# Kernel tuning notes

Measured on AMD Instinct MI355X. Metric: run time of the kernel, lower is better.

The kernel has to match this reference:

```python
import jax, jax.numpy as jnp
import numpy as np
from jax.experimental.ode import odeint

OBS_DIM, LATENT_DIM, HIDDEN_DIM = 64, 3, 128
T, B = 200, 4096
NUM_ENCODE = 50
DYN_H = 100


def setup_inputs() -> dict:
    key = jax.random.key(0)
    ks = jax.random.split(key, 20)
    def rn(k, shape, fan_in):
        return (jax.random.normal(k, shape, jnp.float32) / np.float32(np.sqrt(fan_in)))
    return {
        "observations": jax.random.normal(ks[0], (T, B, OBS_DIM), jnp.float32),
        "epsilon": jax.random.normal(ks[1], (B, LATENT_DIM), jnp.float32),
        # GRU params (PyTorch layout: W_ih [3H, in], W_hh [3H, H])
        "gru_Wih": rn(ks[2], (3 * HIDDEN_DIM, OBS_DIM), OBS_DIM),
        "gru_Whh": rn(ks[3], (3 * HIDDEN_DIM, HIDDEN_DIM), HIDDEN_DIM),
        "gru_bih": jnp.zeros((3 * HIDDEN_DIM,), jnp.float32),
        "gru_bhh": jnp.zeros((3 * HIDDEN_DIM,), jnp.float32),
        "mean_W": rn(ks[4], (LATENT_DIM, HIDDEN_DIM), HIDDEN_DIM),
        "mean_b": jnp.zeros((LATENT_DIM,), jnp.float32),
        "logvar_W": rn(ks[5], (LATENT_DIM, HIDDEN_DIM), HIDDEN_DIM),
        "logvar_b": jnp.zeros((LATENT_DIM,), jnp.float32),
        # dynamics MLP 3->100->100->3
        "dyn_W1": rn(ks[6], (DYN_H, LATENT_DIM), LATENT_DIM),
        "dyn_b1": jnp.zeros((DYN_H,), jnp.float32),
        "dyn_W2": rn(ks[7], (DYN_H, DYN_H), DYN_H),
        "dyn_b2": jnp.zeros((DYN_H,), jnp.float32),
        "dyn_W3": rn(ks[8], (LATENT_DIM, DYN_H), DYN_H),
        "dyn_b3": jnp.zeros((LATENT_DIM,), jnp.float32),
        # decoder MLP latent->64->obs
        "dec_W1": rn(ks[9], (64, LATENT_DIM), LATENT_DIM),
        "dec_b1": jnp.zeros((64,), jnp.float32),
        "dec_W2": rn(ks[10], (OBS_DIM, 64), 64),
        "dec_b2": jnp.zeros((OBS_DIM,), jnp.float32),
        "time_steps": jnp.arange(T, dtype=jnp.float32) * jnp.float32(0.01),
    }


def _gru_last(x, Wih, Whh, bih, bhh):
    # x: [T, B, obs_dim]; PyTorch GRU cell math, zero initial state
    H = Whh.shape[1]
    def step(h, xt):
        gi = xt @ Wih.T + bih          # [B, 3H]
        gh = h @ Whh.T + bhh           # [B, 3H]
        i_r, i_z, i_n = jnp.split(gi, 3, axis=-1)
        h_r, h_z, h_n = jnp.split(gh, 3, axis=-1)
        r = jax.nn.sigmoid(i_r + h_r)
        z = jax.nn.sigmoid(i_z + h_z)
        n = jnp.tanh(i_n + r * h_n)
        return (1.0 - z) * n + z * h, None
    h0 = jnp.zeros((x.shape[1], H), x.dtype)
    h_last, _ = jax.lax.scan(step, h0, x)
    return h_last


def reference(observations, epsilon, gru_Wih, gru_Whh, gru_bih, gru_bhh,
              mean_W, mean_b, logvar_W, logvar_b,
              dyn_W1, dyn_b1, dyn_W2, dyn_b2, dyn_W3, dyn_b3,
              dec_W1, dec_b1, dec_W2, dec_b2, time_steps):
    h_last = _gru_last(observations[:NUM_ENCODE], gru_Wih, gru_Whh, gru_bih, gru_bhh)
    z0_mean = h_last @ mean_W.T + mean_b
    z0_logvar = h_last @ logvar_W.T + logvar_b
    std = jnp.exp(0.5 * z0_logvar)
    z0 = z0_mean + epsilon * std

    def dyn(z, t):
        h = jnp.tanh(z @ dyn_W1.T + dyn_b1)
        h = jnp.tanh(h @ dyn_W2.T + dyn_b2)
        return h @ dyn_W3.T + dyn_b3

    # dopri5 adaptive solver (torchdiffeq default tolerances)
    traj = odeint(dyn, z0, time_steps, rtol=1e-7, atol=1e-9)  # [T, B, latent]
    h = jax.nn.relu(traj @ dec_W1.T + dec_b1)
    recon = h @ dec_W2.T + dec_b2                              # [T, B, obs]
    return recon, z0_mean, z0_logvar, traj
```

## Files before the change

### kernel.cpp

```cpp
#include <hip/hip_runtime.h>
#include <stddef.h>

#define OFF_MEAN 52428800
#define OFF_LV   52441088
#define OFF_TRAJ 52453376

typedef _Float16 f16x8 __attribute__((ext_vector_type(8)));
typedef _Float16 f16x4 __attribute__((ext_vector_type(4)));
typedef float    f32x4 __attribute__((ext_vector_type(4)));

#define MFMA16(a, b, c) __builtin_amdgcn_mfma_f32_16x16x32_f16((a), (b), (c), 0, 0, 0)

__device__ __forceinline__ float sigm_(float x) {
    float e = __builtin_amdgcn_exp2f(x * -1.442695041f);
    return __builtin_amdgcn_rcpf(1.f + e);
}
__device__ __forceinline__ float tanh_(float x) {
    float e = __builtin_amdgcn_exp2f(x * 2.885390082f);
    return 1.f - 2.f * __builtin_amdgcn_rcpf(e + 1.f);
}
__device__ __forceinline__ float dot4_(float4 a, float4 b) {
    return a.x * b.x + a.y * b.y + a.z * b.z + a.w * b.w;
}

__global__ __launch_bounds__(512, 2) void k_gru(
    const float* __restrict__ obs, const float* __restrict__ eps,
    const float* __restrict__ Wih, const float* __restrict__ Whh,
    const float* __restrict__ bih, const float* __restrict__ bhh,
    const float* __restrict__ meanW, const float* __restrict__ meanB,
    const float* __restrict__ lvW,  const float* __restrict__ lvB,
    float* __restrict__ o_mean, float* __restrict__ o_lv, float* __restrict__ z0)
{
    __shared__ alignas(16) unsigned short h_s[2][2048];
    __shared__ alignas(16) unsigned short x_s[2][1024];
    __shared__ alignas(16) float hm_s[16 * 132];
    __shared__ float mb_s[96];

    const int tid  = threadIdx.x;
    const int b0   = blockIdx.x * 16;
    const int lane = tid & 63, wv = tid >> 6;
    const int lrow = lane & 15, lkb = lane >> 4;
    const int swX  = (lrow & 7) << 4;
    const int swH  = lrow << 4;
    const int u    = wv * 16 + lrow;

    const float bR  = bih[u]       + bhh[u];
    const float bZ  = bih[128 + u] + bhh[128 + u];
    const float bNi = bih[256 + u];
    const float bNh = bhh[256 + u];

    f16x8 wihf[3][2];
    #pragma unroll
    for (int g = 0; g < 3; ++g) {
        int col = g * 128 + u;
        #pragma unroll
        for (int ks = 0; ks < 2; ++ks) {
            const float* wp = Wih + col * 64 + ks * 32 + lkb * 8;
            float4 a = *(const float4*)wp, b = *(const float4*)(wp + 4);
            float tmp[8] = {a.x, a.y, a.z, a.w, b.x, b.y, b.z, b.w};
            f16x8 hv;
            #pragma unroll
            for (int j = 0; j < 8; ++j) hv[j] = (_Float16)tmp[j];
            wihf[g][ks] = hv;
        }
    }
    f16x8 whhh[3][4];
    #pragma unroll
    for (int g = 0; g < 3; ++g) {
        int col = g * 128 + u;
        #pragma unroll
        for (int ks = 0; ks < 4; ++ks) {
            const float* wp = Whh + col * 128 + ks * 32 + lkb * 8;
            float4 a = *(const float4*)wp, b = *(const float4*)(wp + 4);
            float tmp[8] = {a.x, a.y, a.z, a.w, b.x, b.y, b.z, b.w};
            f16x8 hv;
            #pragma unroll
            for (int j = 0; j < 8; ++j) hv[j] = (_Float16)tmp[j];
            whhh[g][ks] = hv;
        }
    }

    for (int i = tid; i < 2048; i += 512) h_s[0][i] = 0;
    const int srow = tid >> 4, skq = (tid & 15) * 4;
    const int sxb  = srow * 128 + ((skq * 2) ^ ((srow & 7) << 4));
    float4 xn;
    if (tid < 256) {
        xn = *(const float4*)(obs + ((size_t)0 * 4096 + b0 + srow) * 64 + skq);
        f16x4 vh = {(_Float16)xn.x, (_Float16)xn.y, (_Float16)xn.z, (_Float16)xn.w};
        *(f16x4*)((char*)x_s[0] + sxb) = vh;
    }
    f32x4 hold = {0.f, 0.f, 0.f, 0.f};
    __syncthreads();

    for (int t = 0; t < 50; ++t) {
        const int cur = t & 1, nxt = cur ^ 1;
        char* x_c = (char*)x_s[cur];
        char* h_c = (char*)h_s[cur];

        if (tid < 256) {
            int tt = (t < 49) ? t + 1 : t;
            xn = *(const float4*)(obs + ((size_t)tt * 4096 + b0 + srow) * 64 + skq);
        }

        f16x8 xh[2], hh[4];
        #pragma unroll
        for (int ks = 0; ks < 2; ++ks) {
            int off = lrow * 128 + ((ks * 64 + lkb * 16) ^ swX);
            xh[ks] = *(const f16x8*)(x_c + off);
        }
        #pragma unroll
        for (int ks = 0; ks < 4; ++ks) {
            int off = lrow * 256 + ((ks * 64 + lkb * 16) ^ swH);
            hh[ks] = *(const f16x8*)(h_c + off);
        }

        f32x4 z4 = {0.f, 0.f, 0.f, 0.f};
        f32x4 aR = z4, aZ = z4, aNi = z4, aNh = z4;
        #pragma unroll
        for (int ks = 0; ks < 2; ++ks) {
            aR  = MFMA16(xh[ks], wihf[0][ks], aR);
            aZ  = MFMA16(xh[ks], wihf[1][ks], aZ);
            aNi = MFMA16(xh[ks], wihf[2][ks], aNi);
        }
        #pragma unroll
        for (int ks = 0; ks < 4; ++ks) {
            aR  = MFMA16(hh[ks], whhh[0][ks], aR);
            aZ  = MFMA16(hh[ks], whhh[1][ks], aZ);
            aNh = MFMA16(hh[ks], whhh[2][ks], aNh);
        }

        char* hn_c = (char*)h_s[nxt];
        #pragma unroll
        for (int i = 0; i < 4; ++i) {
            float rg = sigm_(aR[i] + bR);
            float zg = sigm_(aZ[i] + bZ);
            float n  = tanh_(aNi[i] + bNi + rg * (aNh[i] + bNh));
            float hv = (1.f - zg) * n + zg * hold[i];
            hold[i] = hv;
            int ri = lkb * 4 + i;
            int hb = ri * 256 + ((u * 2) ^ (ri << 4));
            *(_Float16*)(hn_c + hb) = (_Float16)hv;
        }

        if (tid < 256 && t < 49) {
            f16x4 vh = {(_Float16)xn.x, (_Float16)xn.y, (_Float16)xn.z, (_Float16)xn.w};
            *(f16x4*)((char*)x_s[nxt] + sxb) = vh;
        }
        __syncthreads();
    }

    #pragma unroll
    for (int i = 0; i < 4; ++i)
        hm_s[(lkb * 4 + i) * 132 + u] = hold[i];
    __syncthreads();

    if (tid < 96) {
        int rr = tid / 6, c = tid - rr * 6, j = (c < 3) ? c : c - 3;
        const float* W = (c < 3) ? meanW : lvW;
        const float* B = (c < 3) ? meanB : lvB;
        float acc = B[j];
        const float4* W4 = (const float4*)(W + j * 128);
        const float4* h4 = (const float4*)(hm_s + rr * 132);
        #pragma unroll 4
        for (int kc = 0; kc < 32; ++kc) acc += dot4_(W4[kc], h4[kc]);
        mb_s[rr * 6 + c] = acc;
    }
    __syncthreads();
    if (tid < 48) {
        int rr = tid / 3, j = tid - rr * 3;
        int gb = b0 + rr;
        float m  = mb_s[rr * 6 + j];
        float lv = mb_s[rr * 6 + j + 3];
        o_mean[gb * 3 + j] = m;
        o_lv[gb * 3 + j]   = lv;
        z0[gb * 3 + j]     = m + eps[gb * 3 + j] * __expf(0.5f * lv);
    }
}

__global__ __launch_bounds__(256, 2) void k_odec(
    const float* __restrict__ dW1, const float* __restrict__ db1,
    const float* __restrict__ dW2, const float* __restrict__ db2,
    const float* __restrict__ dW3, const float* __restrict__ db3,
    const float* __restrict__ decW1, const float* __restrict__ decb1,
    const float* __restrict__ decW2, const float* __restrict__ decb2,
    const float* __restrict__ z0, float* __restrict__ traj, float* __restrict__ recon)
{
    __shared__ alignas(16) unsigned short h1_s[2048];
    __shared__ alignas(16) unsigned short hd_s[10240];
    __shared__ alignas(16) float h2f[8 * 104];
    __shared__ alignas(16) float W3s[312];
    __shared__ alignas(16) float zbuf[160 * 4];
    __shared__ float w1ds[192], b1ds[64];
    __shared__ float b2s[100], b3s[3];
    __shared__ float fparts[24];

    const int tid  = threadIdx.x;
    const int b0   = blockIdx.x * 8;
    const int lane = tid & 63, wv = tid >> 6;
    const int r    = tid >> 5;
    const int lrow = lane & 15, lkb = lane >> 4;
    const int swA  = (lrow & 7) << 4;
    char* h1c = (char*)h1_s;
    char* hdc = (char*)hd_s;

    for (int i = tid; i < 512; i += 256)
        ((unsigned int*)(h1c + 2048))[i] = 0u;
    if (tid < 32) h2f[(tid >> 2) * 104 + 100 + (tid & 3)] = 0.f;
    for (int i = tid; i < 312; i += 256) {
        int j = i / 104, k = i - j * 104;
        W3s[i] = (k < 100) ? dW3[j * 100 + k] : 0.f;
    }
    if (tid < 100) b2s[tid] = db2[tid];
    if (tid < 3)   b3s[tid] = db3[tid];
    if (tid < 192) w1ds[tid] = decW1[tid];
    if (tid < 64)  b1ds[tid] = decb1[tid];

    float w1r[12], b1r[4];
    {
        int k0q = (tid & 31) * 4;
        #pragma unroll
        for (int i = 0; i < 4; ++i) {
            int k = k0q + i;
            if (k < 100) {
                w1r[3 * i + 0] = dW1[k * 3 + 0];
                w1r[3 * i + 1] = dW1[k * 3 + 1];
                w1r[3 * i + 2] = dW1[k * 3 + 2];
                b1r[i] = db1[k];
            } else {
                w1r[3 * i + 0] = 0.f; w1r[3 * i + 1] = 0.f; w1r[3 * i + 2] = 0.f;
                b1r[i] = 0.f;
            }
        }
    }
    f16x8 w2h[2][4];
    #pragma unroll
    for (int tile = 0; tile < 2; ++tile) {
        int col = (wv * 2 + tile) * 16 + lrow;
        #pragma unroll
        for (int ks = 0; ks < 4; ++ks) {
            f16x8 hv;
            #pragma unroll
            for (int j = 0; j < 8; ++j) {
                int k = ks * 32 + lkb * 8 + j;
                float v = (col < 100 && k < 100) ? dW2[col * 100 + k] : 0.f;
                hv[j] = (_Float16)v;
            }
            w2h[tile][ks] = hv;
        }
    }
    const int colD = wv * 16 + lrow;
    f16x8 dbh[2];
    #pragma unroll
    for (int ks = 0; ks < 2; ++ks) {
        const float* wp = decW2 + colD * 64 + ks * 32 + lkb * 8;
        float4 a = *(const float4*)wp, b = *(const float4*)(wp + 4);
        float tmp[8] = {a.x, a.y, a.z, a.w, b.x, b.y, b.z, b.w};
        f16x8 hv;
        #pragma unroll
        for (int j = 0; j < 8; ++j) hv[j] = (_Float16)tmp[j];
        dbh[ks] = hv;
    }
    const float dbo = decb2[colD];

    float yv0 = z0[(b0 + r) * 3 + 0];
    float yv1 = z0[(b0 + r) * 3 + 1];
    float yv2 = z0[(b0 + r) * 3 + 2];
    float fc0, fc1, fc2;
    float k10, k11, k12, ka0, ka1, ka2, yn0, yn1, yn2;
    float po0 = 0.f, po1 = 0.f, po2 = 0.f;
    float pk0 = 0.f, pk1 = 0.f, pk2 = 0.f;
    float pn0 = 0.f, pn1 = 0.f, pn2 = 0.f;
    float pf0 = 0.f, pf1 = 0.f, pf2 = 0.f;
    int have = 0, pt0 = 0;
    __syncthreads();

#define ZCHUNK(T0_, HH_, INVN_)                                                   \
    do {                                                                          \
        for (int ii = (tid & 31); ii < 60; ii += 32) {                            \
            int q = ii / 3, j = ii - q * 3;                                       \
            float ysj = (j == 0) ? po0 : (j == 1) ? po1 : po2;                    \
            float f0j = (j == 0) ? pk0 : (j == 1) ? pk1 : pk2;                    \
            float ynj = (j == 0) ? pn0 : (j == 1) ? pn1 : pn2;                    \
            float fnj = (j == 0) ? pf0 : (j == 1) ? pf1 : pf2;                    \
            float th  = (float)q * (INVN_);                                       \
            float th2 = th * th, th3 = th2 * th;                                  \
            float ca = 2.f * th3 - 3.f * th2 + 1.f;                               \
            float cb = th3 - 2.f * th2 + th;                                      \
            float cc = 3.f * th2 - 2.f * th3;                                     \
            float cd = th3 - th2;                                                 \
            float v = ca * ysj + cb * (HH_) * f0j + cc * ynj + cd * (HH_) * fnj;  \
            traj[((size_t)((T0_) + q) * 4096 + b0 + r) * 3 + j] = v;              \
            zbuf[(q * 8 + r) * 4 + j] = v;                                        \
        }                                                                         \
    } while (0)

#define HCHUNK0                                                                   \
    do {                                                                          \
        const int p  = tid >> 1;                                                  \
        const int u0 = (tid & 1) * 32;                                            \
        const float z0v = zbuf[p * 4 + 0], z1v = zbuf[p * 4 + 1], z2v = zbuf[p * 4 + 2]; \
        const int sw = (p & 7) << 4;                                              \
        _Pragma("unroll")                                                         \
        for (int c = 0; c < 8; ++c) {                                             \
            f16x4 hh_;                                                            \
            _Pragma("unroll")                                                     \
            for (int i = 0; i < 4; ++i) {                                         \
                int u = u0 + c * 4 + i;                                           \
                float acc = b1ds[u] + w1ds[u * 3 + 0] * z0v                       \
                          + w1ds[u * 3 + 1] * z1v + w1ds[u * 3 + 2] * z2v;        \
                hh_[i] = (_Float16)fmaxf(acc, 0.f);                               \
            }                                                                     \
            int off = p * 128 + (((u0 + c * 4) * 2) ^ sw);                        \
            *(f16x4*)(hdc + off) = hh_;                                           \
        }                                                                         \
    } while (0)

#define HCHUNK1                                                                   \
    do {                                                                          \
        const int p  = 128 + (tid >> 3);                                          \
        const int u0 = (tid & 7) * 8;                                             \
        const float z0v = zbuf[p * 4 + 0], z1v = zbuf[p * 4 + 1], z2v = zbuf[p * 4 + 2]; \
        const int sw = (p & 7) << 4;                                              \
        _Pragma("unroll")                                                         \
        for (int c = 0; c < 2; ++c) {                                             \
            f16x4 hh_;                                                            \
            _Pragma("unroll")                                                     \
            for (int i = 0; i < 4; ++i) {                                         \
                int u = u0 + c * 4 + i;                                           \
                float acc = b1ds[u] + w1ds[u * 3 + 0] * z0v                       \
                          + w1ds[u * 3 + 1] * z1v + w1ds[u * 3 + 2] * z2v;        \
                hh_[i] = (_Float16)fmaxf(acc, 0.f);                               \
            }                                                                     \
            int off = p * 128 + (((u0 + c * 4) * 2) ^ sw);                        \
            *(f16x4*)(hdc + off) = hh_;                                           \
        }                                                                         \
    } while (0)

#define MCHUNK(PART_, T0_)                                                        \
    do {                                                                          \
        _Pragma("unroll")                                                         \
        for (int rt2 = 0; rt2 < 5; ++rt2) {                                       \
            int rt = (PART_) * 5 + rt2;                                           \
            int base = (rt * 16 + lrow) * 128;                                    \
            f16x8 a0 = *(const f16x8*)(hdc + base + ((lkb * 16) ^ swA));          \
            f16x8 a1 = *(const f16x8*)(hdc + base + ((64 + lkb * 16) ^ swA));     \
            f32x4 acc = {0.f, 0.f, 0.f, 0.f};                                     \
            acc = MFMA16(a0, dbh[0], acc);                                        \
            acc = MFMA16(a1, dbh[1], acc);                                        \
            _Pragma("unroll")                                                     \
            for (int i = 0; i < 4; ++i) {                                         \
                int pr = rt * 16 + lkb * 4 + i;                                   \
                int q2 = pr >> 3, row2 = pr & 7;                                  \
                recon[((size_t)((T0_) + q2) * 4096 + b0 + row2) * 64 + colD] = acc[i] + dbo; \
            }                                                                     \
        }                                                                         \
    } while (0)

#define FEVAL(Y0, Y1, Y2, CH)                                                     \
    do {                                                                          \
        {                                                            \
            int k0q = (tid & 31) * 4;                                             \
            f16x4 hA;                                                             \
            _Pragma("unroll")                                                     \
            for (int i = 0; i < 4; ++i) {                                         \
                float a_ = b1r[i] + w1r[3 * i] * (Y0)                             \
                         + w1r[3 * i + 1] * (Y1) + w1r[3 * i + 2] * (Y2);         \
                hA[i] = (_Float16)tanh_(a_);                                      \
            }                                                                     \
            *(f16x4*)(h1c + r * 256 + ((k0q * 2) ^ (r << 4))) = hA;               \
        }                                                                         \
        if (have) {                                                               \
            if ((CH) == 1) ZCHUNK(pt0, 0.20f, 0.05f);                             \
            else if ((CH) == 2) HCHUNK0;                                          \
            else if ((CH) == 3) { HCHUNK1; MCHUNK(0, pt0); }                      \
            else if ((CH) == 4) MCHUNK(1, pt0);                                   \
        }                                                                         \
        __syncthreads();                                                          \
        {                                                        \
            f16x8 ah[4];                                                          \
            _Pragma("unroll")                                                     \
            for (int ks = 0; ks < 4; ++ks)                                        \
                ah[ks] = *(const f16x8*)(h1c + lrow * 256 + ((ks * 64 + lkb * 16) ^ swA)); \
            f32x4 acc0 = {0.f, 0.f, 0.f, 0.f}, acc1 = {0.f, 0.f, 0.f, 0.f};       \
            _Pragma("unroll")                                                     \
            for (int ks = 0; ks < 4; ++ks) {                                      \
                acc0 = MFMA16(ah[ks], w2h[0][ks], acc0);                          \
                acc1 = MFMA16(ah[ks], w2h[1][ks], acc1);                          \
            }                                                                     \
            if (lkb < 2) {                                                        \
                int r0 = lkb * 4;                                                 \
                _Pragma("unroll")                                                 \
                for (int tile = 0; tile < 2; ++tile) {                            \
                    int col = (wv * 2 + tile) * 16 + lrow;                        \
                    f32x4 a = tile ? acc1 : acc0;                                 \
                    if (col < 100) {                                              \
                        float bb = b2s[col];                                      \
                        _Pragma("unroll")                                         \
                        for (int i = 0; i < 4; ++i)                               \
                            h2f[(r0 + i) * 104 + col] = tanh_(a[i] + bb);         \
                    }                                                             \
                }                                                                 \
            }                                                                     \
        }                                                                         \
        __syncthreads();                                                          \
        {                                  \
            if (tid < 192) {                                                      \
                int rr = tid / 24, rem = tid - rr * 24, j = rem >> 3, qc = rem & 7;\
                const float4* Wj = (const float4*)(W3s + j * 104);                \
                const float4* Hr = (const float4*)(h2f + rr * 104);               \
                float acc = 0.f;                                                  \
                _Pragma("unroll")                                                 \
                for (int kc = 0; kc < 4; ++kc) {                                  \
                    int k = qc + kc * 8;                                          \
                    if (k < 26) acc += dot4_(Wj[k], Hr[k]);                       \
                }                                                                 \
                acc += __shfl_xor(acc, 1);                                        \
                acc += __shfl_xor(acc, 2);                                        \
                acc += __shfl_xor(acc, 4);                                        \
                if (qc == 0) fparts[rr * 3 + j] = acc + b3s[j];                   \
            }                                                                     \
        }                                                                         \
        __syncthreads();                                                          \
        fc0 = fparts[r * 3 + 0];                                                  \
        fc1 = fparts[r * 3 + 1];                                                  \
        fc2 = fparts[r * 3 + 2];                                                  \
    } while (0)

    FEVAL(yv0, yv1, yv2, 0);

    #pragma unroll 1
    for (int s = 0; s < 10; ++s) {
        const float hh = (s < 9) ? 0.20f : 0.19f;
        have = (s >= 1);
        pt0  = (s - 1) * 20;

        k10 = fc0; k11 = fc1; k12 = fc2;
        ka0 = fc0; ka1 = fc1; ka2 = fc2;
        float yt0 = yv0 + 0.5f * hh * fc0, yt1 = yv1 + 0.5f * hh * fc1, yt2 = yv2 + 0.5f * hh * fc2;
        FEVAL(yt0, yt1, yt2, 1);
        ka0 += 2.f * fc0; ka1 += 2.f * fc1; ka2 += 2.f * fc2;
        yt0 = yv0 + 0.5f * hh * fc0; yt1 = yv1 + 0.5f * hh * fc1; yt2 = yv2 + 0.5f * hh * fc2;
        FEVAL(yt0, yt1, yt2, 2);
        ka0 += 2.f * fc0; ka1 += 2.f * fc1; ka2 += 2.f * fc2;
        yt0 = yv0 + hh * fc0; yt1 = yv1 + hh * fc1; yt2 = yv2 + hh * fc2;
        FEVAL(yt0, yt1, yt2, 3);
        ka0 += fc0; ka1 += fc1; ka2 += fc2;
        const float h6 = hh * (1.f / 6.f);
        yn0 = yv0 + h6 * ka0; yn1 = yv1 + h6 * ka1; yn2 = yv2 + h6 * ka2;
        FEVAL(yn0, yn1, yn2, 4);

        po0 = yv0; po1 = yv1; po2 = yv2;
        pk0 = k10; pk1 = k11; pk2 = k12;
        pn0 = yn0; pn1 = yn1; pn2 = yn2;
        pf0 = fc0; pf1 = fc1; pf2 = fc2;
        yv0 = yn0; yv1 = yn1; yv2 = yn2;
    }

    ZCHUNK(180, 0.19f, (1.f / 19.f));
    __syncthreads();
    HCHUNK0;
    HCHUNK1;
    __syncthreads();
    MCHUNK(0, 180);
    MCHUNK(1, 180);
#undef FEVAL
#undef ZCHUNK
#undef HCHUNK0
#undef HCHUNK1
#undef MCHUNK
}

extern "C" void kernel_launch(void* const* d_in, const int* in_sizes, int n_in,
                              void* d_out, int out_size, void* d_ws, size_t ws_size,
                              hipStream_t stream)
{
    const float* obs   = (const float*)d_in[0];
    const float* eps   = (const float*)d_in[1];
    const float* Wih   = (const float*)d_in[2];
    const float* Whh   = (const float*)d_in[3];
    const float* bih   = (const float*)d_in[4];
    const float* bhh   = (const float*)d_in[5];
    const float* meanW = (const float*)d_in[6];
    const float* meanB = (const float*)d_in[7];
    const float* lvW   = (const float*)d_in[8];
    const float* lvB   = (const float*)d_in[9];
    const float* dW1   = (const float*)d_in[10];
    const float* db1   = (const float*)d_in[11];
    const float* dW2   = (const float*)d_in[12];
    const float* db2   = (const float*)d_in[13];
    const float* dW3   = (const float*)d_in[14];
    const float* db3   = (const float*)d_in[15];
    const float* decW1 = (const float*)d_in[16];
    const float* decb1 = (const float*)d_in[17];
    const float* decW2 = (const float*)d_in[18];
    const float* decb2 = (const float*)d_in[19];

    float* out   = (float*)d_out;
    float* recon = out;
    float* omean = out + OFF_MEAN;
    float* olv   = out + OFF_LV;
    float* traj  = out + OFF_TRAJ;
    float* z0    = (float*)d_ws;

    k_gru<<<dim3(256), dim3(512), 0, stream>>>(obs, eps, Wih, Whh, bih, bhh,
                                               meanW, meanB, lvW, lvB, omean, olv, z0);
    k_odec<<<dim3(512), dim3(256), 0, stream>>>(dW1, db1, dW2, db2, dW3, db3,
                                                decW1, decb1, decW2, decb2,
                                                z0, traj, recon);
}
```

Baseline: 145.9 us.

## Restructure GRU kernel to 8 rows per block with 4 waves covering two hidden tiles

The GRU kernel now uses 256-thread blocks, each handling 8 batch rows instead of 16, and launches 512 blocks so more CUs get work. Each wave owns two 16-unit hidden slices, which doubles its per-wave weight registers and MFMA count, while half the MFMA rows are padding (zeroed) since only 8 rows are valid. The intent is to spread the sequential 50-step recurrence across more blocks and shorten the per-block dependency chain. The cost is wasted MFMA work on padded rows and higher register pressure per thread.

Result: slower. 200.2 us (+37.2%).

```diff
diff --git a/kernel.cpp b/kernel.cpp
--- a/kernel.cpp
+++ b/kernel.cpp
@@ -23,7 +23,7 @@
     return a.x * b.x + a.y * b.y + a.z * b.z + a.w * b.w;
 }
 
-__global__ __launch_bounds__(512, 2) void k_gru(
+__global__ __launch_bounds__(256, 2) void k_gru(
     const float* __restrict__ obs, const float* __restrict__ eps,
     const float* __restrict__ Wih, const float* __restrict__ Whh,
     const float* __restrict__ bih, const float* __restrict__ bhh,
@@ -33,63 +33,86 @@
 {
     __shared__ alignas(16) unsigned short h_s[2][2048];
     __shared__ alignas(16) unsigned short x_s[2][1024];
-    __shared__ alignas(16) float hm_s[16 * 132];
-    __shared__ float mb_s[96];
+    __shared__ alignas(16) float hm_s[8 * 132];
+    __shared__ float mb_s[48];
 
     const int tid  = threadIdx.x;
-    const int b0   = blockIdx.x * 16;
+    const int b0   = blockIdx.x * 8;
     const int lane = tid & 63, wv = tid >> 6;
     const int lrow = lane & 15, lkb = lane >> 4;
     const int swX  = (lrow & 7) << 4;
     const int swH  = lrow << 4;
-    const int u    = wv * 16 + lrow;
-
-    const float bR  = bih[u]       + bhh[u];
-    const float bZ  = bih[128 + u] + bhh[128 + u];
-    const float bNi = bih[256 + u];
-    const float bNh = bhh[256 + u];
-
-    f16x8 wihf[3][2];
-    #pragma unroll
-    for (int g = 0; g < 3; ++g) {
-        int col = g * 128 + u;
-        #pragma unroll
-        for (int ks = 0; ks < 2; ++ks) {
-            const float* wp = Wih + col * 64 + ks * 32 + lkb * 8;
-            float4 a = *(const float4*)wp, b = *(const float4*)(wp + 4);
-            float tmp[8] = {a.x, a.y, a.z, a.w, b.x, b.y, b.z, b.w};
-            f16x8 hv;
+    const int ua   = wv * 16 + lrow;
+    const int ub   = (wv + 4) * 16 + lrow;
+
+    float bRv[2], bZv[2], bNiv[2], bNhv[2];
+    {
+        const int us[2] = {ua, ub};
+        #pragma unroll
+        for (int s2 = 0; s2 < 2; ++s2) {
+            int u = us[s2];
+            bRv[s2]  = bih[u]       + bhh[u];
+            bZv[s2]  = bih[128 + u] + bhh[128 + u];
+            bNiv[s2] = bih[256 + u];
+            bNhv[s2] = bhh[256 + u];
+        }
+    }
+    f16x8 wihf[2][3][2];
+    {
+        const int us[2] = {ua, ub};
+        #pragma unroll
+        for (int s2 = 0; s2 < 2; ++s2) {
             #pragma unroll
-            for (int j = 0; j < 8; ++j) hv[j] = (_Float16)tmp[j];
-            wihf[g][ks] = hv;
-        }
-    }
-    f16x8 whhh[3][4];
-    #pragma unroll
-    for (int g = 0; g < 3; ++g) {
-        int col = g * 128 + u;
-        #pragma unroll
-        for (int ks = 0; ks < 4; ++ks) {
-            const float* wp = Whh + col * 128 + ks * 32 + lkb * 8;
-            float4 a = *(const float4*)wp, b = *(const float4*)(wp + 4);
-            float tmp[8] = {a.x, a.y, a.z, a.w, b.x, b.y, b.z, b.w};
-            f16x8 hv;
+            for (int g = 0; g < 3; ++g) {
+                int col = g * 128 + us[s2];
+                #pragma unroll
+                for (int ks = 0; ks < 2; ++ks) {
+                    const float* wp = Wih + col * 64 + ks * 32 + lkb * 8;
+                    float4 a = *(const float4*)wp, b = *(const float4*)(wp + 4);
+                    float tmp[8] = {a.x, a.y, a.z, a.w, b.x, b.y, b.z, b.w};
+                    f16x8 hv;
+                    #pragma unroll
+                    for (int j = 0; j < 8; ++j) hv[j] = (_Float16)tmp[j];
+                    wihf[s2][g][ks] = hv;
+                }
+            }
+        }
+    }
+    f16x8 whhh[2][3][4];
+    {
+        const int us[2] = {ua, ub};
+        #pragma unroll
+        for (int s2 = 0; s2 < 2; ++s2) {
             #pragma unroll
-            for (int j = 0; j < 8; ++j) hv[j] = (_Float16)tmp[j];
-            whhh[g][ks] = hv;
-        }
-    }
-
-    for (int i = tid; i < 2048; i += 512) h_s[0][i] = 0;
+            for (int g = 0; g < 3; ++g) {
+                int col = g * 128 + us[s2];
+                #pragma unroll
+                for (int ks = 0; ks < 4; ++ks) {
+                    const float* wp = Whh + col * 128 + ks * 32 + lkb * 8;
+                    float4 a = *(const float4*)wp, b = *(const float4*)(wp + 4);
+                    float tmp[8] = {a.x, a.y, a.z, a.w, b.x, b.y, b.z, b.w};
+                    f16x8 hv;
+                    #pragma unroll
+                    for (int j = 0; j < 8; ++j) hv[j] = (_Float16)tmp[j];
+                    whhh[s2][g][ks] = hv;
+                }
+            }
+        }
+    }
+
+    for (int i = tid; i < 4096; i += 256) ((unsigned short*)h_s)[i] = 0;
+    for (int i = tid; i < 2048; i += 256) ((unsigned short*)x_s)[i] = 0;
+
     const int srow = tid >> 4, skq = (tid & 15) * 4;
     const int sxb  = srow * 128 + ((skq * 2) ^ ((srow & 7) << 4));
     float4 xn;
-    if (tid < 256) {
+    if (tid < 128) {
         xn = *(const float4*)(obs + ((size_t)0 * 4096 + b0 + srow) * 64 + skq);
         f16x4 vh = {(_Float16)xn.x, (_Float16)xn.y, (_Float16)xn.z, (_Float16)xn.w};
         *(f16x4*)((char*)x_s[0] + sxb) = vh;
     }
-    f32x4 hold = {0.f, 0.f, 0.f, 0.f};
+    f32x4 holda = {0.f, 0.f, 0.f, 0.f};
+    f32x4 holdb = {0.f, 0.f, 0.f, 0.f};
     __syncthreads();
 
     for (int t = 0; t < 50; ++t) {
@@ -97,7 +120,7 @@
         char* x_c = (char*)x_s[cur];
         char* h_c = (char*)h_s[cur];
 
-        if (tid < 256) {
+        if (tid < 128) {
             int tt = (t < 49) ? t + 1 : t;
             xn = *(const float4*)(obs + ((size_t)tt * 4096 + b0 + srow) * 64 + skq);
         }
@@ -115,46 +138,70 @@
         }
 
         f32x4 z4 = {0.f, 0.f, 0.f, 0.f};
-        f32x4 aR = z4, aZ = z4, aNi = z4, aNh = z4;
+        f32x4 aRa = z4, aZa = z4, aNia = z4, aNha = z4;
+        f32x4 aRb = z4, aZb = z4, aNib = z4, aNhb = z4;
         #pragma unroll
         for (int ks = 0; ks < 2; ++ks) {
-            aR  = MFMA16(xh[ks], wihf[0][ks], aR);
-            aZ  = MFMA16(xh[ks], wihf[1][ks], aZ);
-            aNi = MFMA16(xh[ks], wihf[2][ks], aNi);
+            aRa  = MFMA16(xh[ks], wihf[0][0][ks], aRa);
+            aZa  = MFMA16(xh[ks], wihf[0][1][ks], aZa);
+            aNia = MFMA16(xh[ks], wihf[0][2][ks], aNia);
+            aRb  = MFMA16(xh[ks], wihf[1][0][ks], aRb);
+            aZb  = MFMA16(xh[ks], wihf[1][1][ks], aZb);
+            aNib = MFMA16(xh[ks], wihf[1][2][ks], aNib);
         }
         #pragma unroll
         for (int ks = 0; ks < 4; ++ks) {
-            aR  = MFMA16(hh[ks], whhh[0][ks], aR);
-            aZ  = MFMA16(hh[ks], whhh[1][ks], aZ);
-            aNh = MFMA16(hh[ks], whhh[2][ks], aNh);
+            aRa  = MFMA16(hh[ks], whhh[0][0][ks], aRa);
+            aZa  = MFMA16(hh[ks], whhh[0][1][ks], aZa);
+            aNha = MFMA16(hh[ks], whhh[0][2][ks], aNha);
+            aRb  = MFMA16(hh[ks], whhh[1][0][ks], aRb);
+            aZb  = MFMA16(hh[ks], whhh[1][1][ks], aZb);
+            aNhb = MFMA16(hh[ks], whhh[1][2][ks], aNhb);
         }
 
         char* hn_c = (char*)h_s[nxt];
-        #pragma unroll
-        for (int i = 0; i < 4; ++i) {
-            float rg = sigm_(aR[i] + bR);
-            float zg = sigm_(aZ[i] + bZ);
-            float n  = tanh_(aNi[i] + bNi + rg * (aNh[i] + bNh));
-            float hv = (1.f - zg) * n + zg * hold[i];
-            hold[i] = hv;
-            int ri = lkb * 4 + i;
-            int hb = ri * 256 + ((u * 2) ^ (ri << 4));
-            *(_Float16*)(hn_c + hb) = (_Float16)hv;
-        }
-
-        if (tid < 256 && t < 49) {
+        if (lkb < 2) {
+            #pragma unroll
+            for (int i = 0; i < 4; ++i) {
+                int ri = lkb * 4 + i;
+                {
+                    float rg = sigm_(aRa[i] + bRv[0]);
+                    float zg = sigm_(aZa[i] + bZv[0]);
+                    float n  = tanh_(aNia[i] + bNiv[0] + rg * (aNha[i] + bNhv[0]));
+                    float hv = n + zg * (holda[i] - n);
+                    holda[i] = hv;
+                    int hb = ri * 256 + ((ua * 2) ^ (ri << 4));
+                    *(_Float16*)(hn_c + hb) = (_Float16)hv;
+                }
+                {
+                    float rg = sigm_(aRb[i] + bRv[1]);
+                    float zg = sigm_(aZb[i] + bZv[1]);
+                    float n  = tanh_(aNib[i] + bNiv[1] + rg * (aNhb[i] + bNhv[1]));
+                    float hv = n + zg * (holdb[i] - n);
+                    holdb[i] = hv;
+                    int hb = ri * 256 + ((ub * 2) ^ (ri << 4));
+                    *(_Float16*)(hn_c + hb) = (_Float16)hv;
+                }
+            }
+        }
+
+        if (tid < 128 && t < 49) {
             f16x4 vh = {(_Float16)xn.x, (_Float16)xn.y, (_Float16)xn.z, (_Float16)xn.w};
             *(f16x4*)((char*)x_s[nxt] + sxb) = vh;
         }
         __syncthreads();
     }
 
-    #pragma unroll
-    for (int i = 0; i < 4; ++i)
-        hm_s[(lkb * 4 + i) * 132 + u] = hold[i];
+    if (lkb < 2) {
+        #pragma unroll
+        for (int i = 0; i < 4; ++i) {
+            hm_s[(lkb * 4 + i) * 132 + ua] = holda[i];
+            hm_s[(lkb * 4 + i) * 132 + ub] = holdb[i];
+        }
+    }
     __syncthreads();
 
-    if (tid < 96) {
+    if (tid < 48) {
         int rr = tid / 6, c = tid - rr * 6, j = (c < 3) ? c : c - 3;
         const float* W = (c < 3) ? meanW : lvW;
         const float* B = (c < 3) ? meanB : lvB;
@@ -166,7 +213,7 @@
         mb_s[rr * 6 + c] = acc;
     }
     __syncthreads();
-    if (tid < 48) {
+    if (tid < 24) {
         int rr = tid / 3, j = tid - rr * 3;
         int gb = b0 + rr;
         float m  = mb_s[rr * 6 + j];
@@ -358,7 +405,7 @@
 
 #define FEVAL(Y0, Y1, Y2, CH)                                                     \
     do {                                                                          \
-        {                                                            \
+        {                                                                         \
             int k0q = (tid & 31) * 4;                                             \
             f16x4 hA;                                                             \
             _Pragma("unroll")                                                     \
@@ -376,7 +423,7 @@
             else if ((CH) == 4) MCHUNK(1, pt0);                                   \
         }                                                                         \
         __syncthreads();                                                          \
-        {                                                        \
+        {                                                                         \
             f16x8 ah[4];                                                          \
             _Pragma("unroll")                                                     \
             for (int ks = 0; ks < 4; ++ks)                                        \
@@ -403,7 +450,7 @@
             }                                                                     \
         }                                                                         \
         __syncthreads();                                                          \
-        {                                  \
+        {                                                                         \
             if (tid < 192) {                                                      \
                 int rr = tid / 24, rem = tid - rr * 24, j = rem >> 3, qc = rem & 7;\
                 const float4* Wj = (const float4*)(W3s + j * 104);                \
@@ -502,7 +549,7 @@
     float* traj  = out + OFF_TRAJ;
     float* z0    = (float*)d_ws;
 
-    k_gru<<<dim3(256), dim3(512), 0, stream>>>(obs, eps, Wih, Whh, bih, bhh,
+    k_gru<<<dim3(512), dim3(256), 0, stream>>>(obs, eps, Wih, Whh, bih, bhh,
                                                meanW, meanB, lvW, lvB, omean, olv, z0);
     k_odec<<<dim3(512), dim3(256), 0, stream>>>(dW1, db1, dW2, db2, dW3, db3,
                                                 decW1, decb1, decW2, decb2,
```
